# Kernel tuning notes

Hardware: AMD Instinct MI355X
Metric: run time of the kernel (lower is better)

## Reference

```python
import jax, jax.numpy as jnp
import numpy as np

N = 50000
E = 800000
D_IN = 256
HID = 256
EPS = 1e-12


def _glorot(key, shape):
    fan_in, fan_out = shape[1], shape[0]
    lim = jnp.sqrt(6.0 / (fan_in + fan_out))
    return jax.random.uniform(key, shape, jnp.float32, -lim, lim)


def setup_inputs() -> dict:
    key = jax.random.key(0)
    ks = jax.random.split(key, 8)
    x = jax.random.normal(ks[0], (N, D_IN), jnp.float32)
    edge_index = jax.random.randint(ks[1], (2, E), 0, N, jnp.int64)
    # SAGEConv params: lin_l (neighbor, with bias), lin_r (root, no bias)
    W1l = _glorot(ks[2], (HID, D_IN))
    b1l = jnp.zeros((HID,), jnp.float32)
    W1r = _glorot(ks[3], (HID, D_IN))
    W2l = _glorot(ks[4], (HID, HID))
    b2l = jnp.zeros((HID,), jnp.float32)
    W2r = _glorot(ks[5], (HID, HID))
    return {"x": x, "edge_index": edge_index,
            "W1l": W1l, "b1l": b1l, "W1r": W1r,
            "W2l": W2l, "b2l": b2l, "W2r": W2r}


def _sage_conv(x, src, dst, Wl, bl, Wr, num_nodes):
    # mean aggregation of source features onto destination nodes
    agg = jax.ops.segment_sum(x[src], dst, num_segments=num_nodes)          # [N, d]
    cnt = jax.ops.segment_sum(jnp.ones((src.shape[0],), x.dtype), dst,
                              num_segments=num_nodes)                        # [N]
    mean = agg / jnp.maximum(cnt, 1.0)[:, None]
    out = mean @ Wl.T + bl + x @ Wr.T                                        # [N, out]
    # L2 normalize (normalize=True)
    norm = jnp.linalg.norm(out, axis=-1, keepdims=True)
    return out / jnp.maximum(norm, EPS)


def reference(x, edge_index, W1l, b1l, W1r, W2l, b2l, W2r):
    src, dst = edge_index[0], edge_index[1]
    n = x.shape[0]
    h = _sage_conv(x, src, dst, W1l, b1l, W1r, n)
    h = jax.nn.relu(h)
    h = _sage_conv(h, src, dst, W2l, b2l, W2r, n)
    return h
```

## Files before the change

kernel.cpp:

```cpp
#include <hip/hip_runtime.h>
#include <hip/hip_bf16.h>


#define DD 256
#define NPB 128
#define CSRCAP 2048

typedef unsigned short ushort_t;
using bf16x8 = __attribute__((ext_vector_type(8))) short;
using f32x4  = __attribute__((ext_vector_type(4))) float;
using i32x4  = __attribute__((ext_vector_type(4))) int;

static __device__ __forceinline__ float b2f(ushort_t u) {
    __hip_bfloat16 h = *reinterpret_cast<__hip_bfloat16*>(&u);
    return __bfloat162float(h);
}
static __device__ __forceinline__ ushort_t f2b(float f) {
    __hip_bfloat16 h = __float2bfloat16(f);
    return *reinterpret_cast<ushort_t*>(&h);
}

static __device__ __forceinline__ void load16(const ushort_t* g, ushort_t* l) {
    __builtin_amdgcn_global_load_lds(
        (const __attribute__((address_space(1))) unsigned*)(g),
        (__attribute__((address_space(3))) unsigned*)(l),
        16, 0, 0);
}

static __device__ __forceinline__ size_t sma(int npad, int node, int col) {
    return ((size_t)(col >> 5) * npad + node) * 32 + (col & 31);
}


__global__ __launch_bounds__(256) void prep_kernel(
        const int* __restrict__ ei, int* __restrict__ cnt, int E, int eb,
        const float* __restrict__ x, ushort_t* __restrict__ xb, int xe, int cxb,
        int npad,
        const float* __restrict__ w1l, const float* __restrict__ w1r,
        const float* __restrict__ w2l, const float* __restrict__ w2r,
        ushort_t* __restrict__ wc1, ushort_t* __restrict__ wc2) {
    int b = blockIdx.x;
    if (b < eb) {
        int e = b * 256 + threadIdx.x;
        if (e < E) atomicAdd(&cnt[ei[E + e]], 1);
        return;
    }
    b -= eb;
    if (b < cxb) {
        int i = (b * 256 + threadIdx.x) * 8;
        if (i + 8 > xe) return;
        int node = i >> 8, col = i & 255;
        float4 a = *(const float4*)(x + i);
        float4 c = *(const float4*)(x + i + 4);
        ushort_t o[8] = {f2b(a.x), f2b(a.y), f2b(a.z), f2b(a.w),
                         f2b(c.x), f2b(c.y), f2b(c.z), f2b(c.w)};
        *(i32x4*)(xb + sma(npad, node, col)) = *(const i32x4*)o;
        return;
    }
    b -= cxb;
    {
        int i = (b * 256 + threadIdx.x) * 8;
        int which = i >> 16;
        int o = i & 65535;
        int row = o >> 8, col = o & 255;
        const float* src = (which == 0) ? w1l : (which == 1) ? w1r
                          : (which == 2) ? w2l : w2r;
        ushort_t* dst = ((which < 2) ? wc1 : wc2)
                        + (size_t)row * 512 + (which & 1) * 256 + col;
        float4 a = *(const float4*)(src + o);
        float4 c = *(const float4*)(src + o + 4);
        ushort_t ov[8] = {f2b(a.x), f2b(a.y), f2b(a.z), f2b(a.w),
                          f2b(c.x), f2b(c.y), f2b(c.z), f2b(c.w)};
        *(i32x4*)dst = *(const i32x4*)ov;
    }
}


__global__ __launch_bounds__(256) void scan_partial_kernel(const int* __restrict__ cnt,
                                                           int* __restrict__ part, int n) {
    __shared__ int ws[4];
    int tid = threadIdx.x;
    int wave = tid >> 6, lane = tid & 63;
    int i0 = blockIdx.x * 2048 + tid * 8;
    int sum = 0;
    if (i0 + 8 <= n) {
        int4 a = *(const int4*)(cnt + i0);
        int4 b = *(const int4*)(cnt + i0 + 4);
        sum = a.x + a.y + a.z + a.w + b.x + b.y + b.z + b.w;
    } else {
        for (int j = i0; j < n; j++) sum += cnt[j];
    }
    #pragma unroll
    for (int off = 1; off < 64; off <<= 1) sum += __shfl_xor(sum, off);
    if (lane == 0) ws[wave] = sum;
    __syncthreads();
    if (tid == 0) part[blockIdx.x] = ws[0] + ws[1] + ws[2] + ws[3];
}

__global__ __launch_bounds__(256) void scan_final_kernel(const int* __restrict__ cnt,
                                                         const int* __restrict__ part,
                                                         int* __restrict__ offs,
                                                         int* __restrict__ bcur,
                                                         int n, int E, int nb) {
    __shared__ int wt[4];
    __shared__ int sbase;
    int tid = threadIdx.x;
    int wave = tid >> 6, lane = tid & 63;
    if (tid < 64) {
        int pv = (tid < nb) ? part[tid] : 0;
        int incl = pv;
        #pragma unroll
        for (int off = 1; off < 64; off <<= 1) {
            int t = __shfl_up(incl, off);
            if (tid >= off) incl += t;
        }
        if (tid == (int)blockIdx.x) sbase = incl - pv;
    }
    int i0 = blockIdx.x * 2048 + tid * 8;
    int v[8], s[8];
    int run = 0;
    if (i0 + 8 <= n) {
        int4 a = *(const int4*)(cnt + i0);
        int4 b = *(const int4*)(cnt + i0 + 4);
        v[0] = a.x; v[1] = a.y; v[2] = a.z; v[3] = a.w;
        v[4] = b.x; v[5] = b.y; v[6] = b.z; v[7] = b.w;
    } else {
        #pragma unroll
        for (int j = 0; j < 8; j++) v[j] = (i0 + j < n) ? cnt[i0 + j] : 0;
    }
    #pragma unroll
    for (int j = 0; j < 8; j++) { run += v[j]; s[j] = run; }
    int tsum = run;
    int incl = tsum;
    #pragma unroll
    for (int off = 1; off < 64; off <<= 1) {
        int t = __shfl_up(incl, off);
        if (lane >= off) incl += t;
    }
    if (lane == 63) wt[wave] = incl;
    __syncthreads();
    int woff = 0;
    for (int w = 0; w < wave; w++) woff += wt[w];
    int texcl = sbase + woff + (incl - tsum);
    #pragma unroll
    for (int j = 0; j < 8; j++) {
        int idx = i0 + j;
        if (idx < n) {
            int e = texcl + s[j] - v[j];
            offs[idx] = e;
            if ((idx & (NPB - 1)) == 0) bcur[idx / NPB] = e;
        }
    }
    if (blockIdx.x == 0 && tid == 0) offs[n] = E;
}


__global__ __launch_bounds__(256) void part_kernel(const int* __restrict__ ei,
                                                   int* __restrict__ bcur,
                                                   int2* __restrict__ stage,
                                                   int E, int nbuck) {
    __shared__ int hist[512];
    __shared__ int gbase[512];
    int tid = threadIdx.x;
    for (int i = tid; i < nbuck; i += 256) hist[i] = 0;
    __syncthreads();
    int sv[8], dv[8], bk[8], rk[8];
    #pragma unroll
    for (int j = 0; j < 8; j++) {
        int e = blockIdx.x * 2048 + j * 256 + tid;
        if (e < E) {
            sv[j] = ei[e];
            dv[j] = ei[E + e];
            bk[j] = dv[j] / NPB;
            rk[j] = atomicAdd(&hist[bk[j]], 1);
        } else bk[j] = -1;
    }
    __syncthreads();
    for (int i = tid; i < nbuck; i += 256) {
        int h = hist[i];
        gbase[i] = h ? atomicAdd(&bcur[i], h) : 0;
    }
    __syncthreads();
    #pragma unroll
    for (int j = 0; j < 8; j++)
        if (bk[j] >= 0) {
            int p = gbase[bk[j]] + rk[j];
            stage[p] = make_int2(sv[j], dv[j]);
        }
}

__global__ __launch_bounds__(256) void group_kernel(const int2* __restrict__ stage,
                                                    const int* __restrict__ offs,
                                                    int* __restrict__ csr, int N) {
    __shared__ int lcur[NPB];
    int b = blockIdx.x;
    int lo = b * NPB;
    int hi = min(N, lo + NPB);
    int tid = threadIdx.x;
    if (tid < hi - lo) lcur[tid] = offs[lo + tid];
    __syncthreads();
    int base = offs[lo];
    int m = offs[hi] - base;
    for (int t = tid; t < m; t += 256) {
        int2 v = stage[base + t];
        int p = atomicAdd(&lcur[v.y - lo], 1);
        csr[p] = v.x;
    }
}


static __device__ __forceinline__ void add8(float* acc, i32x4 v) {
    const unsigned* u = (const unsigned*)&v;
    #pragma unroll
    for (int j = 0; j < 4; j++) {
        acc[2 * j]     += __uint_as_float(u[j] << 16);
        acc[2 * j + 1] += __uint_as_float(u[j] & 0xffff0000u);
    }
}

__global__ __launch_bounds__(256) void agg_kernel(const ushort_t* __restrict__ F,
                                                  const int* __restrict__ csr,
                                                  const int* __restrict__ offs,
                                                  ushort_t* __restrict__ mean,
                                                  int N, int npad) {
    __shared__ int lidx[CSRCAP];
    __shared__ int soffs[65];
    int s = blockIdx.x & 7;
    int g0 = (blockIdx.x >> 3) * 64;
    int tid = threadIdx.x;
    int gcnt = min(N - g0, 64);
    if (tid <= gcnt) soffs[tid] = offs[g0 + tid];
    __syncthreads();
    int base = soffs[0];
    int total = soffs[gcnt] - base;
    int stg = min(total, CSRCAP);
    for (int i = tid; i < stg; i += 256) lidx[i] = csr[base + i];
    __syncthreads();

    int node = tid >> 2, ch = tid & 3;
    if (node >= gcnt) return;
    const ushort_t* Fs = F + ((size_t)s * npad) * 32 + ch * 8;
    int beg = soffs[node] - base, end = soffs[node + 1] - base;

    float acc[8];
    #pragma unroll
    for (int j = 0; j < 8; j++) acc[j] = 0.f;

    if (total <= CSRCAP) {
        int i = beg;
        for (; i + 4 <= end; i += 4) {
            i32x4 v0 = *(const i32x4*)(Fs + (size_t)lidx[i]     * 32);
            i32x4 v1 = *(const i32x4*)(Fs + (size_t)lidx[i + 1] * 32);
            i32x4 v2 = *(const i32x4*)(Fs + (size_t)lidx[i + 2] * 32);
            i32x4 v3 = *(const i32x4*)(Fs + (size_t)lidx[i + 3] * 32);
            add8(acc, v0); add8(acc, v1); add8(acc, v2); add8(acc, v3);
        }
        for (; i < end; i++) {
            i32x4 v = *(const i32x4*)(Fs + (size_t)lidx[i] * 32);
            add8(acc, v);
        }
    } else {
        for (int i = beg; i < end; i++) {
            i32x4 v = *(const i32x4*)(Fs + (size_t)csr[base + i] * 32);
            add8(acc, v);
        }
    }

    float scale = 1.f / fmaxf((float)(end - beg), 1.f);
    ushort_t o[8];
    #pragma unroll
    for (int j = 0; j < 8; j++) o[j] = f2b(acc[j] * scale);
    *(i32x4*)(mean + ((size_t)s * npad + g0 + node) * 32 + ch * 8) = *(const i32x4*)o;
}


__global__ __launch_bounds__(512, 4) void gemm_norm_kernel(
        const ushort_t* __restrict__ meanb,
        const ushort_t* __restrict__ fb,
        const ushort_t* __restrict__ W,
        const float*    __restrict__ bias,
        ushort_t* __restrict__ outb,
        float*    __restrict__ outf,
        int npad, int N, int relu) {
    __shared__ union {
        struct {
            ushort_t As[128 * 64];
            ushort_t Bs[256 * 64];
        } s;
        ushort_t ebuf[64 * 264];
    } u;
    __shared__ float rowsq[128];

    int tid = threadIdx.x;
    int wave = tid >> 6, lane = tid & 63;
    int quad = lane >> 4, m16 = lane & 15;
    int swz = m16 & 7;
    int rowhalf = wave >> 2;
    int colq = wave & 3;
    int rowbase = blockIdx.x * 128;

    if (tid < 128) rowsq[tid] = 0.f;

    f32x4 acc[4][4];
    #pragma unroll
    for (int i = 0; i < 4; i++)
        #pragma unroll
        for (int j = 0; j < 4; j++)
            acc[i][j] = (f32x4){0.f, 0.f, 0.f, 0.f};

    for (int ki = 0; ki < 8; ki++) {
        int kb = ki * 64;
        const ushort_t* Ab = (ki < 4) ? meanb : fb;
        int kl = kb & 255;
        __syncthreads();
        #pragma unroll
        for (int t = 0; t < 2; t++) {
            int instr = wave * 2 + t;
            int flat = instr * 64 + lane;
            int row = flat >> 3, cc = flat & 7;
            int ccg = cc ^ (row & 7);
            int c = kl + ccg * 8;
            load16(Ab + sma(npad, rowbase + row, c), &u.s.As[instr * 512]);
        }
        #pragma unroll
        for (int t = 0; t < 4; t++) {
            int instr = wave * 4 + t;
            int flat = instr * 64 + lane;
            int row = flat >> 3, cc = flat & 7;
            int ccg = cc ^ (row & 7);
            load16(W + (size_t)row * 512 + kb + ccg * 8, &u.s.Bs[instr * 512]);
        }
        __syncthreads();

        #pragma unroll
        for (int ks = 0; ks < 2; ks++) {
            int cbase = ks * 4 + quad;
            bf16x8 af[4], bfr[4];
            #pragma unroll
            for (int rt = 0; rt < 4; rt++) {
                int r = rowhalf * 64 + rt * 16 + m16;
                af[rt] = *(const bf16x8*)&u.s.As[r * 64 + ((cbase ^ swz)) * 8];
            }
            #pragma unroll
            for (int ct = 0; ct < 4; ct++) {
                int r = colq * 64 + ct * 16 + m16;
                bfr[ct] = *(const bf16x8*)&u.s.Bs[r * 64 + ((cbase ^ swz)) * 8];
            }
            #pragma unroll
            for (int rt = 0; rt < 4; rt++)
                #pragma unroll
                for (int ct = 0; ct < 4; ct++)
                    acc[rt][ct] = __builtin_amdgcn_mfma_f32_16x16x32_bf16(
                        af[rt], bfr[ct], acc[rt][ct], 0, 0, 0);
        }
    }

    float bvals[4];
    #pragma unroll
    for (int ct = 0; ct < 4; ct++)
        bvals[ct] = bias[colq * 64 + ct * 16 + m16];
    #pragma unroll
    for (int rt = 0; rt < 4; rt++) {
        #pragma unroll
        for (int reg = 0; reg < 4; reg++) {
            float s = 0.f;
            #pragma unroll
            for (int ct = 0; ct < 4; ct++) {
                float v = acc[rt][ct][reg] + bvals[ct];
                acc[rt][ct][reg] = v;
                s += v * v;
            }
            #pragma unroll
            for (int off = 1; off < 16; off <<= 1)
                s += __shfl_xor(s, off);
            if (m16 == 0)
                atomicAdd(&rowsq[rowhalf * 64 + rt * 16 + quad * 4 + reg], s);
        }
    }
    __syncthreads();

    #pragma unroll
    for (int p = 0; p < 2; p++) {
        if (rowhalf == p) {
            #pragma unroll
            for (int rt = 0; rt < 4; rt++) {
                #pragma unroll
                for (int reg = 0; reg < 4; reg++) {
                    int rl = rt * 16 + quad * 4 + reg;
                    float inv = 1.f / fmaxf(sqrtf(rowsq[p * 64 + rl]), 1e-12f);
                    #pragma unroll
                    for (int ct = 0; ct < 4; ct++) {
                        float v = acc[rt][ct][reg] * inv;
                        if (relu) v = fmaxf(v, 0.f);
                        int col = colq * 64 + ct * 16 + m16;
                        u.ebuf[rl * 264 + col] = f2b(v);
                    }
                }
            }
        }
        __syncthreads();
        #pragma unroll
        for (int j = 0; j < 4; j++) {
            int flat = j * 512 + tid;
            int row = flat >> 5, cc = flat & 31;
            int gr = rowbase + p * 64 + row;
            if (gr < N) {
                bf16x8 v = *(const bf16x8*)&u.ebuf[row * 264 + cc * 8];
                if (outf) {
                    float4 f0, f1;
                    f0.x = b2f((ushort_t)v[0]); f0.y = b2f((ushort_t)v[1]);
                    f0.z = b2f((ushort_t)v[2]); f0.w = b2f((ushort_t)v[3]);
                    f1.x = b2f((ushort_t)v[4]); f1.y = b2f((ushort_t)v[5]);
                    f1.z = b2f((ushort_t)v[6]); f1.w = b2f((ushort_t)v[7]);
                    float* ptr = outf + (size_t)gr * 256 + cc * 8;
                    *(float4*)ptr = f0;
                    *(float4*)(ptr + 4) = f1;
                } else {
                    *(bf16x8*)(outb + sma(npad, gr, cc * 8)) = v;
                }
            }
        }
        __syncthreads();
    }
}


static inline size_t align_up(size_t x, size_t a) { return (x + a - 1) & ~(a - 1); }

extern "C" void kernel_launch(void* const* d_in, const int* in_sizes, int n_in,
                              void* d_out, int out_size, void* d_ws, size_t ws_size,
                              hipStream_t stream) {
    const float* x   = (const float*)d_in[0];
    const int*   ei  = (const int*)d_in[1];
    const float* W1l = (const float*)d_in[2];
    const float* b1l = (const float*)d_in[3];
    const float* W1r = (const float*)d_in[4];
    const float* W2l = (const float*)d_in[5];
    const float* b2l = (const float*)d_in[6];
    const float* W2r = (const float*)d_in[7];

    int N = in_sizes[0] / DD;
    int E = in_sizes[1] / 2;
    int npad = N + 128;
    int nbuck = (N + NPB - 1) / NPB;

    char* ws = (char*)d_ws;
    size_t off = 0;
    int* cnt = (int*)(ws + off);      off = align_up(off + (size_t)N * 4, 256);
    int* offs = (int*)(ws + off);     off = align_up(off + (size_t)(N + 1) * 4, 256);
    int* bcur = (int*)(ws + off);     off = align_up(off + (size_t)512 * 4, 256);
    int* part = (int*)(ws + off);     off = align_up(off + (size_t)64 * 4, 256);
    int* csr = (int*)(ws + off);      off = align_up(off + (size_t)E * 4, 256);
    size_t sstage = off;
    int2* stage = (int2*)(ws + sstage);
    size_t meansz = (size_t)npad * 32 * 8 * 2;
    off = align_up(sstage + ((size_t)E * 8 > meansz ? (size_t)E * 8 : meansz), 256);
    ushort_t* meanb = (ushort_t*)(ws + sstage);
    ushort_t* xb = (ushort_t*)(ws + off);  off = align_up(off + meansz, 256);
    ushort_t* hb = (ushort_t*)(ws + off);  off = align_up(off + meansz, 256);
    ushort_t* wc1 = (ushort_t*)(ws + off); off = align_up(off + (size_t)256 * 512 * 2, 256);
    ushort_t* wc2 = (ushort_t*)(ws + off); off = align_up(off + (size_t)256 * 512 * 2, 256);

    hipMemsetAsync(cnt, 0, (size_t)N * 4, stream);

    int xe = N * DD;
    int eb = (E + 255) / 256;
    int cxb = (xe / 8 + 255) / 256;
    int cwb = (4 * DD * DD / 8) / 256;
    prep_kernel<<<eb + cxb + cwb, 256, 0, stream>>>(ei, cnt, E, eb,
                                                    x, xb, xe, cxb, npad,
                                                    W1l, W1r, W2l, W2r, wc1, wc2);

    int nb = (N + 2047) / 2048;
    scan_partial_kernel<<<nb, 256, 0, stream>>>(cnt, part, N);
    scan_final_kernel<<<nb, 256, 0, stream>>>(cnt, part, offs, bcur, N, E, nb);

    int pb = (E + 2047) / 2048;
    part_kernel<<<pb, 256, 0, stream>>>(ei, bcur, stage, E, nbuck);
    group_kernel<<<nbuck, 256, 0, stream>>>(stage, offs, csr, N);

    int ab = 8 * ((N + 63) / 64);
    int gb = (N + 127) / 128;

    agg_kernel<<<ab, 256, 0, stream>>>(xb, csr, offs, meanb, N, npad);
    gemm_norm_kernel<<<gb, 512, 0, stream>>>(meanb, xb, wc1, b1l,
                                             hb, (float*)nullptr, npad, N, 1);

    agg_kernel<<<ab, 256, 0, stream>>>(hb, csr, offs, meanb, N, npad);
    gemm_norm_kernel<<<gb, 512, 0, stream>>>(meanb, hb, wc2, b2l,
                                             (ushort_t*)nullptr, (float*)d_out, npad, N, 0);
}
```

Baseline: 308.0 us.

## Count edges per bucket instead of per node and build offsets in group kernel

Edge degree counting in the prep kernel now runs per 128-node bucket through a shared-memory histogram, replacing 800k global atomics on per-node counters. The two-kernel per-node prefix scan becomes a single-block scan over at most 512 bucket counts. Per-node degrees and CSR offsets are computed inside group_kernel with a local histogram and scan. This removes one kernel launch and many global atomics, at the cost of a second pass over the staged edges in group_kernel.

```diff
diff --git a/kernel.cpp b/kernel.cpp
--- a/kernel.cpp
+++ b/kernel.cpp
@@ -33,21 +33,33 @@
 
 
 __global__ __launch_bounds__(256) void prep_kernel(
-        const int* __restrict__ ei, int* __restrict__ cnt, int E, int eb,
+        const int* __restrict__ ei, int* __restrict__ bcnt, int E, int eb2,
         const float* __restrict__ x, ushort_t* __restrict__ xb, int xe, int cxb,
         int npad,
         const float* __restrict__ w1l, const float* __restrict__ w1r,
         const float* __restrict__ w2l, const float* __restrict__ w2r,
         ushort_t* __restrict__ wc1, ushort_t* __restrict__ wc2) {
     int b = blockIdx.x;
-    if (b < eb) {
-        int e = b * 256 + threadIdx.x;
-        if (e < E) atomicAdd(&cnt[ei[E + e]], 1);
+    int tid = threadIdx.x;
+    if (b < eb2) {
+        __shared__ int hist[512];
+        for (int i = tid; i < 512; i += 256) hist[i] = 0;
+        __syncthreads();
+        #pragma unroll
+        for (int j = 0; j < 8; j++) {
+            int e = b * 2048 + j * 256 + tid;
+            if (e < E) atomicAdd(&hist[ei[E + e] >> 7], 1);
+        }
+        __syncthreads();
+        for (int i = tid; i < 512; i += 256) {
+            int h = hist[i];
+            if (h) atomicAdd(&bcnt[i], h);
+        }
         return;
     }
-    b -= eb;
+    b -= eb2;
     if (b < cxb) {
-        int i = (b * 256 + threadIdx.x) * 8;
+        int i = (b * 256 + tid) * 8;
         if (i + 8 > xe) return;
         int node = i >> 8, col = i & 255;
         float4 a = *(const float4*)(x + i);
@@ -59,7 +71,7 @@
     }
     b -= cxb;
     {
-        int i = (b * 256 + threadIdx.x) * 8;
+        int i = (b * 256 + tid) * 8;
         int which = i >> 16;
         int o = i & 65535;
         int row = o >> 8, col = o & 255;
@@ -76,62 +88,15 @@
 }
 
 
-__global__ __launch_bounds__(256) void scan_partial_kernel(const int* __restrict__ cnt,
-                                                           int* __restrict__ part, int n) {
-    __shared__ int ws[4];
+__global__ __launch_bounds__(512) void bucket_scan_kernel(
+        const int* __restrict__ bcnt, int* __restrict__ bbase,
+        int* __restrict__ bcur, int* __restrict__ offs,
+        int nbuck, int N, int E) {
+    __shared__ int wt[8];
     int tid = threadIdx.x;
     int wave = tid >> 6, lane = tid & 63;
-    int i0 = blockIdx.x * 2048 + tid * 8;
-    int sum = 0;
-    if (i0 + 8 <= n) {
-        int4 a = *(const int4*)(cnt + i0);
-        int4 b = *(const int4*)(cnt + i0 + 4);
-        sum = a.x + a.y + a.z + a.w + b.x + b.y + b.z + b.w;
-    } else {
-        for (int j = i0; j < n; j++) sum += cnt[j];
-    }
-    #pragma unroll
-    for (int off = 1; off < 64; off <<= 1) sum += __shfl_xor(sum, off);
-    if (lane == 0) ws[wave] = sum;
-    __syncthreads();
-    if (tid == 0) part[blockIdx.x] = ws[0] + ws[1] + ws[2] + ws[3];
-}
-
-__global__ __launch_bounds__(256) void scan_final_kernel(const int* __restrict__ cnt,
-                                                         const int* __restrict__ part,
-                                                         int* __restrict__ offs,
-                                                         int* __restrict__ bcur,
-                                                         int n, int E, int nb) {
-    __shared__ int wt[4];
-    __shared__ int sbase;
-    int tid = threadIdx.x;
-    int wave = tid >> 6, lane = tid & 63;
-    if (tid < 64) {
-        int pv = (tid < nb) ? part[tid] : 0;
-        int incl = pv;
-        #pragma unroll
-        for (int off = 1; off < 64; off <<= 1) {
-            int t = __shfl_up(incl, off);
-            if (tid >= off) incl += t;
-        }
-        if (tid == (int)blockIdx.x) sbase = incl - pv;
-    }
-    int i0 = blockIdx.x * 2048 + tid * 8;
-    int v[8], s[8];
-    int run = 0;
-    if (i0 + 8 <= n) {
-        int4 a = *(const int4*)(cnt + i0);
-        int4 b = *(const int4*)(cnt + i0 + 4);
-        v[0] = a.x; v[1] = a.y; v[2] = a.z; v[3] = a.w;
-        v[4] = b.x; v[5] = b.y; v[6] = b.z; v[7] = b.w;
-    } else {
-        #pragma unroll
-        for (int j = 0; j < 8; j++) v[j] = (i0 + j < n) ? cnt[i0 + j] : 0;
-    }
-    #pragma unroll
-    for (int j = 0; j < 8; j++) { run += v[j]; s[j] = run; }
-    int tsum = run;
-    int incl = tsum;
+    int c = (tid < nbuck) ? bcnt[tid] : 0;
+    int incl = c;
     #pragma unroll
     for (int off = 1; off < 64; off <<= 1) {
         int t = __shfl_up(incl, off);
@@ -141,17 +106,9 @@
     __syncthreads();
     int woff = 0;
     for (int w = 0; w < wave; w++) woff += wt[w];
-    int texcl = sbase + woff + (incl - tsum);
-    #pragma unroll
-    for (int j = 0; j < 8; j++) {
-        int idx = i0 + j;
-        if (idx < n) {
-            int e = texcl + s[j] - v[j];
-            offs[idx] = e;
-            if ((idx & (NPB - 1)) == 0) bcur[idx / NPB] = e;
-        }
-    }
-    if (blockIdx.x == 0 && tid == 0) offs[n] = E;
+    int excl = woff + incl - c;
+    if (tid < nbuck) { bbase[tid] = excl; bcur[tid] = excl; }
+    if (tid == 0) offs[N] = E;
 }
 
 
@@ -190,21 +147,41 @@
 }
 
 __global__ __launch_bounds__(256) void group_kernel(const int2* __restrict__ stage,
-                                                    const int* __restrict__ offs,
+                                                    const int* __restrict__ bbase,
+                                                    const int* __restrict__ bcnt,
+                                                    int* __restrict__ offs,
                                                     int* __restrict__ csr, int N) {
-    __shared__ int lcur[NPB];
+    __shared__ int ldeg[NPB];
+    __shared__ int lpos[NPB];
+    __shared__ int wsum;
     int b = blockIdx.x;
     int lo = b * NPB;
-    int hi = min(N, lo + NPB);
-    int tid = threadIdx.x;
-    if (tid < hi - lo) lcur[tid] = offs[lo + tid];
-    __syncthreads();
-    int base = offs[lo];
-    int m = offs[hi] - base;
+    int gcnt = min(N - lo, NPB);
+    int tid = threadIdx.x;
+    if (tid < NPB) ldeg[tid] = 0;
+    __syncthreads();
+    int base = bbase[b];
+    int m = bcnt[b];
+    for (int t = tid; t < m; t += 256)
+        atomicAdd(&ldeg[stage[base + t].y - lo], 1);
+    __syncthreads();
+    int v = (tid < NPB) ? ldeg[tid] : 0;
+    int incl = v;
+    #pragma unroll
+    for (int off = 1; off < 64; off <<= 1) {
+        int t = __shfl_up(incl, off);
+        if ((tid & 63) >= off) incl += t;
+    }
+    if (tid == 63) wsum = incl;
+    __syncthreads();
+    int excl = incl - v + ((tid >= 64 && tid < NPB) ? wsum : 0);
+    if (tid < NPB) lpos[tid] = base + excl;
+    if (tid < gcnt) offs[lo + tid] = base + excl;
+    __syncthreads();
     for (int t = tid; t < m; t += 256) {
-        int2 v = stage[base + t];
-        int p = atomicAdd(&lcur[v.y - lo], 1);
-        csr[p] = v.x;
+        int2 e = stage[base + t];
+        int p = atomicAdd(&lpos[e.y - lo], 1);
+        csr[p] = e.x;
     }
 }
 
@@ -446,10 +423,10 @@
 
     char* ws = (char*)d_ws;
     size_t off = 0;
-    int* cnt = (int*)(ws + off);      off = align_up(off + (size_t)N * 4, 256);
+    int* bcnt = (int*)(ws + off);     off = align_up(off + (size_t)512 * 4, 256);
+    int* bbase = (int*)(ws + off);    off = align_up(off + (size_t)512 * 4, 256);
+    int* bcur = (int*)(ws + off);     off = align_up(off + (size_t)512 * 4, 256);
     int* offs = (int*)(ws + off);     off = align_up(off + (size_t)(N + 1) * 4, 256);
-    int* bcur = (int*)(ws + off);     off = align_up(off + (size_t)512 * 4, 256);
-    int* part = (int*)(ws + off);     off = align_up(off + (size_t)64 * 4, 256);
     int* csr = (int*)(ws + off);      off = align_up(off + (size_t)E * 4, 256);
     size_t sstage = off;
     int2* stage = (int2*)(ws + sstage);
@@ -461,23 +438,21 @@
     ushort_t* wc1 = (ushort_t*)(ws + off); off = align_up(off + (size_t)256 * 512 * 2, 256);
     ushort_t* wc2 = (ushort_t*)(ws + off); off = align_up(off + (size_t)256 * 512 * 2, 256);
 
-    hipMemsetAsync(cnt, 0, (size_t)N * 4, stream);
+    hipMemsetAsync(bcnt, 0, (size_t)512 * 4, stream);
 
     int xe = N * DD;
-    int eb = (E + 255) / 256;
+    int eb2 = (E + 2047) / 2048;
     int cxb = (xe / 8 + 255) / 256;
     int cwb = (4 * DD * DD / 8) / 256;
-    prep_kernel<<<eb + cxb + cwb, 256, 0, stream>>>(ei, cnt, E, eb,
-                                                    x, xb, xe, cxb, npad,
-                                                    W1l, W1r, W2l, W2r, wc1, wc2);
-
-    int nb = (N + 2047) / 2048;
-    scan_partial_kernel<<<nb, 256, 0, stream>>>(cnt, part, N);
-    scan_final_kernel<<<nb, 256, 0, stream>>>(cnt, part, offs, bcur, N, E, nb);
+    prep_kernel<<<eb2 + cxb + cwb, 256, 0, stream>>>(ei, bcnt, E, eb2,
+                                                     x, xb, xe, cxb, npad,
+                                                     W1l, W1r, W2l, W2r, wc1, wc2);
+
+    bucket_scan_kernel<<<1, 512, 0, stream>>>(bcnt, bbase, bcur, offs, nbuck, N, E);
 
     int pb = (E + 2047) / 2048;
     part_kernel<<<pb, 256, 0, stream>>>(ei, bcur, stage, E, nbuck);
-    group_kernel<<<nbuck, 256, 0, stream>>>(stage, offs, csr, N);
+    group_kernel<<<nbuck, 256, 0, stream>>>(stage, bbase, bcnt, offs, csr, N);
 
     int ab = 8 * ((N + 63) / 64);
     int gb = (N + 127) / 128;
```

After: 279.2 us. -9.3%, faster.
